# Performance work log

Measured on AMD Instinct MI355X. Metric: run time of the kernel, lower is better.

## Reference

```python
import jax, jax.numpy as jnp
import numpy as np

LX = LZ = 64
B_BOND = 8
KCH = 3
DX = DZ = 2
N_STATES = 4
SAMPLES = 65536


def setup_inputs() -> dict:
    key = jax.random.key(0)
    k1, k2, k3, k4 = jax.random.split(key, 4)
    biadj = jax.random.normal(k1, (LX, LZ, B_BOND), dtype=jnp.float32)
    eps_ten = jax.random.normal(k2, (B_BOND, KCH, DX, DZ), dtype=jnp.float32)
    chi = jax.random.normal(k3, (N_STATES, N_STATES, KCH), dtype=jnp.float32)
    x0_idx = jax.random.randint(k4, (SAMPLES, LX * DX), 0, N_STATES)
    return {"biadj": biadj, "eps_ten": eps_ten, "chi": chi, "x0_idx": x0_idx}


def _kernel(biadj, eps_ten, chi):
    # biadj: [Lx,Lz,b], eps_ten: [b,k,dx,dz], chi: [n,n,k]
    Lx, Lz, _ = biadj.shape
    _, k, dx, dz = eps_ten.shape
    coupling = jnp.tensordot(biadj, eps_ten, axes=([2], [0]))  # [Lx,Lz,k,dx,dz]
    coupling = coupling.transpose(0, 3, 1, 4, 2).reshape(Lx * dx, Lz * dz, k)
    return jnp.tensordot(coupling, chi, axes=([2], [2]))  # [X,Z,n,n]


def reference(biadj, eps_ten, chi, x0_idx):
    """ERBM.cd_x with steps=1: one Gibbs sweep + CD loss. Returns (loss, x)."""
    n = chi.shape[0]
    K = _kernel(biadj, eps_ten, chi)  # [X,Z,n,n]
    x0 = jax.nn.one_hot(x0_idx, n, dtype=K.dtype)  # [S,X,n]
    kz, kx = jax.random.split(jax.random.key(42))
    # ez = tensordot(x0, K, dims=([1,2],[0,2])) -> [S,Z,n]
    ez = jnp.einsum('sxa,xzab->szb', x0, K)
    z = jax.nn.one_hot(jax.random.categorical(kz, -ez), n, dtype=K.dtype)
    # ex = tensordot(z, K, dims=([1,2],[1,3])) -> [S,X,n]
    ex = jnp.einsum('szb,xzab->sxa', z, K)
    x = jax.nn.one_hot(jax.random.categorical(kx, -ex), n, dtype=K.dtype)
    loss = jnp.sum(ex * (x0 - x), axis=(1, 2)).mean()
    return loss, x
```

## Files before the change

kernel.cpp:

```cpp
#include <hip/hip_runtime.h>
#include <stdint.h>

#define NS   65536
#define XD   128
#define ZD   128

struct U2 { uint32_t x, y; };

__host__ __device__ constexpr uint32_t rotl32(uint32_t v, int r) {
  return (v << r) | (v >> (32 - r));
}

__host__ __device__ constexpr U2 threefry2x32(uint32_t k0, uint32_t k1,
                                              uint32_t x0, uint32_t x1) {
  uint32_t ks0 = k0, ks1 = k1, ks2 = k0 ^ k1 ^ 0x1BD11BDAu;
  x0 += ks0; x1 += ks1;
  x0 += x1; x1 = rotl32(x1, 13); x1 ^= x0;
  x0 += x1; x1 = rotl32(x1, 15); x1 ^= x0;
  x0 += x1; x1 = rotl32(x1, 26); x1 ^= x0;
  x0 += x1; x1 = rotl32(x1,  6); x1 ^= x0;
  x0 += ks1; x1 += ks2 + 1u;
  x0 += x1; x1 = rotl32(x1, 17); x1 ^= x0;
  x0 += x1; x1 = rotl32(x1, 29); x1 ^= x0;
  x0 += x1; x1 = rotl32(x1, 16); x1 ^= x0;
  x0 += x1; x1 = rotl32(x1, 24); x1 ^= x0;
  x0 += ks2; x1 += ks0 + 2u;
  x0 += x1; x1 = rotl32(x1, 13); x1 ^= x0;
  x0 += x1; x1 = rotl32(x1, 15); x1 ^= x0;
  x0 += x1; x1 = rotl32(x1, 26); x1 ^= x0;
  x0 += x1; x1 = rotl32(x1,  6); x1 ^= x0;
  x0 += ks0; x1 += ks1 + 3u;
  x0 += x1; x1 = rotl32(x1, 17); x1 ^= x0;
  x0 += x1; x1 = rotl32(x1, 29); x1 ^= x0;
  x0 += x1; x1 = rotl32(x1, 16); x1 ^= x0;
  x0 += x1; x1 = rotl32(x1, 24); x1 ^= x0;
  x0 += ks1; x1 += ks2 + 4u;
  x0 += x1; x1 = rotl32(x1, 13); x1 ^= x0;
  x0 += x1; x1 = rotl32(x1, 15); x1 ^= x0;
  x0 += x1; x1 = rotl32(x1, 26); x1 ^= x0;
  x0 += x1; x1 = rotl32(x1,  6); x1 ^= x0;
  x0 += ks2; x1 += ks0 + 5u;
  return {x0, x1};
}

constexpr U2 KEYZ = threefry2x32(0u, 42u, 0u, 0u);
constexpr U2 KEYX = threefry2x32(0u, 42u, 0u, 1u);
constexpr uint32_t KZ0 = KEYZ.x, KZ1 = KEYZ.y;
constexpr uint32_t KX0 = KEYX.x, KX1 = KEYX.y;

__device__ inline float gumbel32f(uint32_t k0, uint32_t k1, uint32_t idx) {
  U2 h = threefry2x32(k0, k1, 0u, idx);
  uint32_t bits = h.x ^ h.y;
  float f = __uint_as_float((bits >> 9) | 0x3f800000u) - 1.0f;
  float u = fmaxf(f, 1.1754943508222875e-38f);
  float lu = __logf(u);
  return -__logf(-lu);
}

__global__ __launch_bounds__(256) void pack_x0(const int* __restrict__ x0,
                                               uint32_t* __restrict__ pk,
                                               double* __restrict__ loss_acc) {
  int t = blockIdx.x * 256 + threadIdx.x;
  if (t == 0) *loss_acc = 0.0;
  const int4* src = (const int4*)x0 + (size_t)t * 4;
  uint32_t w = 0;
#pragma unroll
  for (int i = 0; i < 4; ++i) {
    int4 v = src[i];
    w |= (uint32_t)(v.x & 3) << (8 * i + 0);
    w |= (uint32_t)(v.y & 3) << (8 * i + 2);
    w |= (uint32_t)(v.z & 3) << (8 * i + 4);
    w |= (uint32_t)(v.w & 3) << (8 * i + 6);
  }
  pk[t] = w;
}

__global__ __launch_bounds__(256) void build_k(const float* __restrict__ biadj,
                                               const float* __restrict__ eps,
                                               const float* __restrict__ chi,
                                               float* __restrict__ Kz,
                                               float* __restrict__ Kx) {
  int t = blockIdx.x * 256 + threadIdx.x;
  int xx = t >> 7, zz = t & 127;
  int ix = xx >> 1, dx = xx & 1;
  int iz = zz >> 1, dz = zz & 1;
  double c0 = 0.0, c1 = 0.0, c2 = 0.0;
#pragma unroll
  for (int b = 0; b < 8; ++b) {
    double bi = (double)biadj[(ix * 64 + iz) * 8 + b];
    c0 += bi * (double)eps[((b * 3 + 0) * 2 + dx) * 2 + dz];
    c1 += bi * (double)eps[((b * 3 + 1) * 2 + dx) * 2 + dz];
    c2 += bi * (double)eps[((b * 3 + 2) * 2 + dx) * 2 + dz];
  }
#pragma unroll
  for (int p = 0; p < 4; ++p)
#pragma unroll
    for (int q = 0; q < 4; ++q) {
      double kv = c0 * (double)chi[(p * 4 + q) * 3 + 0]
                + c1 * (double)chi[(p * 4 + q) * 3 + 1]
                + c2 * (double)chi[(p * 4 + q) * 3 + 2];
      float kf = (float)kv;
      Kz[((zz * 128 + xx) * 4 + p) * 4 + q] = kf;
      Kx[((xx * 128 + zz) * 4 + q) * 4 + p] = kf;
    }
}

__global__ __launch_bounds__(256) void build_pairs(const float* __restrict__ Kz,
                                                   const float* __restrict__ Kx,
                                                   float4* __restrict__ PZ,
                                                   float4* __restrict__ PX) {
  int gid = blockIdx.x * 256 + threadIdx.x;
  int isX = gid >> 17;
  int t = gid & 131071;
  int c = t & 15, rp = (t >> 4) & 63, r = t >> 10;
  const float4* K4 = (const float4*)(isX ? Kx : Kz);
  float4 kA = K4[(r * 128 + 2 * rp) * 4 + (c & 3)];
  float4 kB = K4[(r * 128 + 2 * rp + 1) * 4 + (c >> 2)];
  float4* P = isX ? PX : PZ;
  P[(r * 64 + rp) * 16 + c] =
      float4{kA.x + kB.x, kA.y + kB.y, kA.z + kB.z, kA.w + kB.w};
}

__device__ inline void pair_accum2(const float4* __restrict__ L,
                                   const uint32_t* __restrict__ cw,
                                   double* __restrict__ dA,
                                   double* __restrict__ dB) {
#pragma unroll
  for (int g = 0; g < 4; ++g) {
    float a0 = 0.f, a1 = 0.f, a2 = 0.f, a3 = 0.f;
    float b0 = 0.f, b1 = 0.f, b2 = 0.f, b3 = 0.f;
#pragma unroll
    for (int j2 = 0; j2 < 2; ++j2) {
      uint32_t w = cw[2 * g + j2];
#pragma unroll
      for (int t = 0; t < 8; ++t) {
        int c = (w >> (4 * t)) & 15;
        const float4* e = &L[(16 * g + 8 * j2 + t) * 16 + c];
        float4 e0 = e[0];
        float4 e1 = e[1024];
        a0 += e0.x; a1 += e0.y; a2 += e0.z; a3 += e0.w;
        b0 += e1.x; b1 += e1.y; b2 += e1.z; b3 += e1.w;
      }
    }
    dA[0] += (double)a0; dA[1] += (double)a1; dA[2] += (double)a2; dA[3] += (double)a3;
    dB[0] += (double)b0; dB[1] += (double)b1; dB[2] += (double)b2; dB[3] += (double)b3;
  }
}

__device__ inline int argmax4(double v0, double v1, double v2, double v3) {
  int best = 0; double bv = v0;
  if (v1 > bv) { bv = v1; best = 1; }
  if (v2 > bv) { bv = v2; best = 2; }
  if (v3 > bv) { bv = v3; best = 3; }
  return best;
}

__global__ __launch_bounds__(256, 4) void ez_pair(const float4* __restrict__ PZ,
                                                  const uint32_t* __restrict__ pk,
                                                  uint8_t* __restrict__ zidxT) {
  __shared__ float4 Ltab[2048];
  int tid = threadIdx.x;
  int by = blockIdx.y;
  {
    const uint4* src = (const uint4*)(PZ + (size_t)by * 2048);
    uint4* dst = (uint4*)Ltab;
#pragma unroll
    for (int i = 0; i < 8; ++i) dst[tid + i * 256] = src[tid + i * 256];
  }
  __syncthreads();
  int s = blockIdx.x * 256 + tid;
  uint32_t cw[8];
  {
    uint4 w0 = *(const uint4*)(pk + (size_t)s * 8);
    uint4 w1 = *(const uint4*)(pk + (size_t)s * 8 + 4);
    cw[0] = w0.x; cw[1] = w0.y; cw[2] = w0.z; cw[3] = w0.w;
    cw[4] = w1.x; cw[5] = w1.y; cw[6] = w1.z; cw[7] = w1.w;
  }
  double dA[4] = {0, 0, 0, 0}, dB[4] = {0, 0, 0, 0};
  pair_accum2(Ltab, cw, dA, dB);

  int z0 = 2 * by, z1 = 2 * by + 1;
  uint32_t ibA = ((uint32_t)s * 128u + (uint32_t)z0) * 4u;
  int bestA = argmax4((double)gumbel32f(KZ0, KZ1, ibA + 0u) - dA[0],
                      (double)gumbel32f(KZ0, KZ1, ibA + 1u) - dA[1],
                      (double)gumbel32f(KZ0, KZ1, ibA + 2u) - dA[2],
                      (double)gumbel32f(KZ0, KZ1, ibA + 3u) - dA[3]);
  uint32_t ibB = ibA + 4u;
  int bestB = argmax4((double)gumbel32f(KZ0, KZ1, ibB + 0u) - dB[0],
                      (double)gumbel32f(KZ0, KZ1, ibB + 1u) - dB[1],
                      (double)gumbel32f(KZ0, KZ1, ibB + 2u) - dB[2],
                      (double)gumbel32f(KZ0, KZ1, ibB + 3u) - dB[3]);
  zidxT[(size_t)z0 * NS + s] = (uint8_t)bestA;
  zidxT[(size_t)z1 * NS + s] = (uint8_t)bestB;
}

__global__ __launch_bounds__(256) void repack_z(const uint8_t* __restrict__ zidxT,
                                                uint32_t* __restrict__ zpk) {
  uint32_t t = blockIdx.x * 256u + threadIdx.x;
  uint32_t j = t >> 16, s = t & 65535u;
  uint32_t w = 0;
#pragma unroll
  for (int k = 0; k < 16; ++k)
    w |= (uint32_t)zidxT[(size_t)(16 * j + k) * NS + s] << (2 * k);
  zpk[t] = w;
}

__global__ __launch_bounds__(256, 4) void ex_pair(const float4* __restrict__ PX,
                                                  const uint32_t* __restrict__ zpk,
                                                  const uint32_t* __restrict__ pk,
                                                  uint8_t* __restrict__ xidxT,
                                                  double* __restrict__ loss_acc) {
  __shared__ float4 Ltab[2048];
  __shared__ double red[4];
  int tid = threadIdx.x;
  int by = blockIdx.y;
  {
    const uint4* src = (const uint4*)(PX + (size_t)by * 2048);
    uint4* dst = (uint4*)Ltab;
#pragma unroll
    for (int i = 0; i < 8; ++i) dst[tid + i * 256] = src[tid + i * 256];
  }
  __syncthreads();
  int s = blockIdx.x * 256 + tid;
  uint32_t cw[8];
#pragma unroll
  for (int j = 0; j < 8; ++j) cw[j] = zpk[(size_t)j * NS + s];
  double dA[4] = {0, 0, 0, 0}, dB[4] = {0, 0, 0, 0};
  pair_accum2(Ltab, cw, dA, dB);

  int x0 = 2 * by, x1 = 2 * by + 1;
  uint32_t ibA = ((uint32_t)s * 128u + (uint32_t)x0) * 4u;
  int bestA = argmax4((double)gumbel32f(KX0, KX1, ibA + 0u) - dA[0],
                      (double)gumbel32f(KX0, KX1, ibA + 1u) - dA[1],
                      (double)gumbel32f(KX0, KX1, ibA + 2u) - dA[2],
                      (double)gumbel32f(KX0, KX1, ibA + 3u) - dA[3]);
  uint32_t ibB = ibA + 4u;
  int bestB = argmax4((double)gumbel32f(KX0, KX1, ibB + 0u) - dB[0],
                      (double)gumbel32f(KX0, KX1, ibB + 1u) - dB[1],
                      (double)gumbel32f(KX0, KX1, ibB + 2u) - dB[2],
                      (double)gumbel32f(KX0, KX1, ibB + 3u) - dB[3]);
  xidxT[(size_t)x0 * NS + s] = (uint8_t)bestA;
  xidxT[(size_t)x1 * NS + s] = (uint8_t)bestB;

  uint32_t wj = pk[(size_t)s * 8 + (x0 >> 4)];
  int aiA = (wj >> (2 * (x0 & 15))) & 3;
  int aiB = (wj >> (2 * (x1 & 15))) & 3;
  double term =
      ((aiA == 0) ? dA[0] : (aiA == 1) ? dA[1] : (aiA == 2) ? dA[2] : dA[3]) -
      ((bestA == 0) ? dA[0] : (bestA == 1) ? dA[1] : (bestA == 2) ? dA[2] : dA[3]) +
      ((aiB == 0) ? dB[0] : (aiB == 1) ? dB[1] : (aiB == 2) ? dB[2] : dB[3]) -
      ((bestB == 0) ? dB[0] : (bestB == 1) ? dB[1] : (bestB == 2) ? dB[2] : dB[3]);
#pragma unroll
  for (int off = 32; off > 0; off >>= 1) term += __shfl_down(term, off, 64);
  int wid = tid >> 6;
  if ((tid & 63) == 0) red[wid] = term;
  __syncthreads();
  if (tid == 0) atomicAdd(loss_acc, red[0] + red[1] + red[2] + red[3]);
}

__global__ __launch_bounds__(256) void write_out(const uint8_t* __restrict__ xidxT,
                                                 const double* __restrict__ loss_acc,
                                                 float* __restrict__ out) {
  __shared__ uint8_t tile[128 * 80];
  int tid = threadIdx.x;
  int s0 = blockIdx.x * 64;
  {
    int x = tid >> 1, chunk = tid & 1;
    const uint8_t* src = xidxT + (size_t)x * NS + s0 + chunk * 32;
    uint4 v0 = *(const uint4*)(src);
    uint4 v1 = *(const uint4*)(src + 16);
    *(uint4*)&tile[x * 80 + chunk * 32 + 0]  = v0;
    *(uint4*)&tile[x * 80 + chunk * 32 + 16] = v1;
  }
  __syncthreads();
  float* dst = out + 1 + (size_t)s0 * 512;
#pragma unroll 4
  for (int k = 0; k < 128; ++k) {
    int f = k * 256 + tid;
    int c = f & 3, x = (f >> 2) & 127, sl = f >> 9;
    uint8_t b = tile[x * 80 + sl];
    dst[f] = (c == (int)b) ? 1.0f : 0.0f;
  }
  if (blockIdx.x == 0 && tid == 0) out[0] = (float)(*loss_acc * (1.0 / 65536.0));
}

extern "C" void kernel_launch(void* const* d_in, const int* in_sizes, int n_in,
                              void* d_out, int out_size, void* d_ws, size_t ws_size,
                              hipStream_t stream) {
  const float* biadj = (const float*)d_in[0];
  const float* eps   = (const float*)d_in[1];
  const float* chi   = (const float*)d_in[2];
  const int*   x0    = (const int*)d_in[3];
  float* out = (float*)d_out;

  char* w = (char*)d_ws;
  double*   loss_acc = (double*)w;                 w += 256;
  float*    Kz    = (float*)w;                     w += (size_t)128 * 128 * 16 * 4;
  float*    Kx    = (float*)w;                     w += (size_t)128 * 128 * 16 * 4;
  uint32_t* pk    = (uint32_t*)w;                  w += (size_t)NS * 8 * 4;
  uint8_t*  zidxT = (uint8_t*)w;                   w += (size_t)NS * ZD;
  uint32_t* zpk   = (uint32_t*)w;                  w += (size_t)NS * 8 * 4;
  uint8_t*  xidxT = (uint8_t*)w;                   w += (size_t)NS * XD;
  float4*   PZ    = (float4*)w;                    w += (size_t)128 * 64 * 16 * 16;
  float4*   PX    = (float4*)w;

  pack_x0<<<NS * 8 / 256, 256, 0, stream>>>(x0, pk, loss_acc);
  build_k<<<64, 256, 0, stream>>>(biadj, eps, chi, Kz, Kx);
  build_pairs<<<1024, 256, 0, stream>>>(Kz, Kx, PZ, PX);
  ez_pair<<<dim3(NS / 256, ZD / 2), 256, 0, stream>>>(PZ, pk, zidxT);
  repack_z<<<NS * 8 / 256, 256, 0, stream>>>(zidxT, zpk);
  ex_pair<<<dim3(NS / 256, XD / 2), 256, 0, stream>>>(PX, zpk, pk, xidxT, loss_acc);
  write_out<<<NS / 64, 256, 0, stream>>>(xidxT, loss_acc, out);
}
```

Baseline: 540.4 us.

## Process two samples per thread in pair kernels and fuse init kernels

The ez_pair and ex_pair kernels now handle two samples per thread, halving the grid so each block's shared-memory table load is amortized over twice as many samples. The x0 packing and K building kernels are merged into one launch, and the per-block loss reduction now does one atomic per wavefront instead of a shared-memory sync. This adds register pressure from doubled accumulators, and the min-blocks hint is raised to 5, which could cause spills, and more contended double atomics.

```diff
diff --git a/kernel.cpp b/kernel.cpp
--- a/kernel.cpp
+++ b/kernel.cpp
@@ -57,52 +57,53 @@
   return -__logf(-lu);
 }
 
-__global__ __launch_bounds__(256) void pack_x0(const int* __restrict__ x0,
-                                               uint32_t* __restrict__ pk,
-                                               double* __restrict__ loss_acc) {
-  int t = blockIdx.x * 256 + threadIdx.x;
-  if (t == 0) *loss_acc = 0.0;
-  const int4* src = (const int4*)x0 + (size_t)t * 4;
-  uint32_t w = 0;
-#pragma unroll
-  for (int i = 0; i < 4; ++i) {
-    int4 v = src[i];
-    w |= (uint32_t)(v.x & 3) << (8 * i + 0);
-    w |= (uint32_t)(v.y & 3) << (8 * i + 2);
-    w |= (uint32_t)(v.z & 3) << (8 * i + 4);
-    w |= (uint32_t)(v.w & 3) << (8 * i + 6);
-  }
-  pk[t] = w;
-}
-
-__global__ __launch_bounds__(256) void build_k(const float* __restrict__ biadj,
-                                               const float* __restrict__ eps,
-                                               const float* __restrict__ chi,
-                                               float* __restrict__ Kz,
-                                               float* __restrict__ Kx) {
-  int t = blockIdx.x * 256 + threadIdx.x;
-  int xx = t >> 7, zz = t & 127;
-  int ix = xx >> 1, dx = xx & 1;
-  int iz = zz >> 1, dz = zz & 1;
-  double c0 = 0.0, c1 = 0.0, c2 = 0.0;
-#pragma unroll
-  for (int b = 0; b < 8; ++b) {
-    double bi = (double)biadj[(ix * 64 + iz) * 8 + b];
-    c0 += bi * (double)eps[((b * 3 + 0) * 2 + dx) * 2 + dz];
-    c1 += bi * (double)eps[((b * 3 + 1) * 2 + dx) * 2 + dz];
-    c2 += bi * (double)eps[((b * 3 + 2) * 2 + dx) * 2 + dz];
-  }
-#pragma unroll
-  for (int p = 0; p < 4; ++p)
-#pragma unroll
-    for (int q = 0; q < 4; ++q) {
-      double kv = c0 * (double)chi[(p * 4 + q) * 3 + 0]
-                + c1 * (double)chi[(p * 4 + q) * 3 + 1]
-                + c2 * (double)chi[(p * 4 + q) * 3 + 2];
-      float kf = (float)kv;
-      Kz[((zz * 128 + xx) * 4 + p) * 4 + q] = kf;
-      Kx[((xx * 128 + zz) * 4 + q) * 4 + p] = kf;
+__global__ __launch_bounds__(256) void init_fused(const int* __restrict__ x0,
+                                                  const float* __restrict__ biadj,
+                                                  const float* __restrict__ eps,
+                                                  const float* __restrict__ chi,
+                                                  uint32_t* __restrict__ pk,
+                                                  float* __restrict__ Kz,
+                                                  float* __restrict__ Kx,
+                                                  double* __restrict__ loss_acc) {
+  if (blockIdx.x < 2048) {
+    int t = blockIdx.x * 256 + threadIdx.x;
+    if (t == 0) *loss_acc = 0.0;
+    const int4* src = (const int4*)x0 + (size_t)t * 4;
+    uint32_t w = 0;
+#pragma unroll
+    for (int i = 0; i < 4; ++i) {
+      int4 v = src[i];
+      w |= (uint32_t)(v.x & 3) << (8 * i + 0);
+      w |= (uint32_t)(v.y & 3) << (8 * i + 2);
+      w |= (uint32_t)(v.z & 3) << (8 * i + 4);
+      w |= (uint32_t)(v.w & 3) << (8 * i + 6);
     }
+    pk[t] = w;
+  } else {
+    int t = (blockIdx.x - 2048) * 256 + threadIdx.x;
+    int xx = t >> 7, zz = t & 127;
+    int ix = xx >> 1, dx = xx & 1;
+    int iz = zz >> 1, dz = zz & 1;
+    double c0 = 0.0, c1 = 0.0, c2 = 0.0;
+#pragma unroll
+    for (int b = 0; b < 8; ++b) {
+      double bi = (double)biadj[(ix * 64 + iz) * 8 + b];
+      c0 += bi * (double)eps[((b * 3 + 0) * 2 + dx) * 2 + dz];
+      c1 += bi * (double)eps[((b * 3 + 1) * 2 + dx) * 2 + dz];
+      c2 += bi * (double)eps[((b * 3 + 2) * 2 + dx) * 2 + dz];
+    }
+#pragma unroll
+    for (int p = 0; p < 4; ++p)
+#pragma unroll
+      for (int q = 0; q < 4; ++q) {
+        double kv = c0 * (double)chi[(p * 4 + q) * 3 + 0]
+                  + c1 * (double)chi[(p * 4 + q) * 3 + 1]
+                  + c2 * (double)chi[(p * 4 + q) * 3 + 2];
+        float kf = (float)kv;
+        Kz[((zz * 128 + xx) * 4 + p) * 4 + q] = kf;
+        Kx[((xx * 128 + zz) * 4 + q) * 4 + p] = kf;
+      }
+  }
 }
 
 __global__ __launch_bounds__(256) void build_pairs(const float* __restrict__ Kz,
@@ -121,29 +122,43 @@
       float4{kA.x + kB.x, kA.y + kB.y, kA.z + kB.z, kA.w + kB.w};
 }
 
-__device__ inline void pair_accum2(const float4* __restrict__ L,
-                                   const uint32_t* __restrict__ cw,
-                                   double* __restrict__ dA,
-                                   double* __restrict__ dB) {
+__device__ inline void pair_accum4(const float4* __restrict__ L,
+                                   const uint32_t* __restrict__ cw0,
+                                   const uint32_t* __restrict__ cw1,
+                                   double* __restrict__ d0A, double* __restrict__ d0B,
+                                   double* __restrict__ d1A, double* __restrict__ d1B) {
 #pragma unroll
   for (int g = 0; g < 4; ++g) {
-    float a0 = 0.f, a1 = 0.f, a2 = 0.f, a3 = 0.f;
-    float b0 = 0.f, b1 = 0.f, b2 = 0.f, b3 = 0.f;
+    float a0[4] = {0.f, 0.f, 0.f, 0.f};
+    float b0[4] = {0.f, 0.f, 0.f, 0.f};
+    float a1[4] = {0.f, 0.f, 0.f, 0.f};
+    float b1[4] = {0.f, 0.f, 0.f, 0.f};
 #pragma unroll
     for (int j2 = 0; j2 < 2; ++j2) {
-      uint32_t w = cw[2 * g + j2];
+      uint32_t w0 = cw0[2 * g + j2];
+      uint32_t w1 = cw1[2 * g + j2];
 #pragma unroll
       for (int t = 0; t < 8; ++t) {
-        int c = (w >> (4 * t)) & 15;
-        const float4* e = &L[(16 * g + 8 * j2 + t) * 16 + c];
-        float4 e0 = e[0];
-        float4 e1 = e[1024];
-        a0 += e0.x; a1 += e0.y; a2 += e0.z; a3 += e0.w;
-        b0 += e1.x; b1 += e1.y; b2 += e1.z; b3 += e1.w;
+        int base = (16 * g + 8 * j2 + t) * 16;
+        int c0 = (w0 >> (4 * t)) & 15;
+        int c1 = (w1 >> (4 * t)) & 15;
+        const float4* e0 = &L[base + c0];
+        const float4* e1 = &L[base + c1];
+        float4 e00 = e0[0];
+        float4 e01 = e0[1024];
+        float4 e10 = e1[0];
+        float4 e11 = e1[1024];
+        a0[0] += e00.x; a0[1] += e00.y; a0[2] += e00.z; a0[3] += e00.w;
+        b0[0] += e01.x; b0[1] += e01.y; b0[2] += e01.z; b0[3] += e01.w;
+        a1[0] += e10.x; a1[1] += e10.y; a1[2] += e10.z; a1[3] += e10.w;
+        b1[0] += e11.x; b1[1] += e11.y; b1[2] += e11.z; b1[3] += e11.w;
       }
     }
-    dA[0] += (double)a0; dA[1] += (double)a1; dA[2] += (double)a2; dA[3] += (double)a3;
-    dB[0] += (double)b0; dB[1] += (double)b1; dB[2] += (double)b2; dB[3] += (double)b3;
+#pragma unroll
+    for (int k = 0; k < 4; ++k) {
+      d0A[k] += (double)a0[k]; d0B[k] += (double)b0[k];
+      d1A[k] += (double)a1[k]; d1B[k] += (double)b1[k];
+    }
   }
 }
 
@@ -155,7 +170,15 @@
   return best;
 }
 
-__global__ __launch_bounds__(256, 4) void ez_pair(const float4* __restrict__ PZ,
+__device__ inline int sample4(uint32_t k0, uint32_t k1, uint32_t ib,
+                              const double* d) {
+  return argmax4((double)gumbel32f(k0, k1, ib + 0u) - d[0],
+                 (double)gumbel32f(k0, k1, ib + 1u) - d[1],
+                 (double)gumbel32f(k0, k1, ib + 2u) - d[2],
+                 (double)gumbel32f(k0, k1, ib + 3u) - d[3]);
+}
+
+__global__ __launch_bounds__(256, 5) void ez_pair(const float4* __restrict__ PZ,
                                                   const uint32_t* __restrict__ pk,
                                                   uint8_t* __restrict__ zidxT) {
   __shared__ float4 Ltab[2048];
@@ -168,30 +191,30 @@
     for (int i = 0; i < 8; ++i) dst[tid + i * 256] = src[tid + i * 256];
   }
   __syncthreads();
-  int s = blockIdx.x * 256 + tid;
-  uint32_t cw[8];
+  int s0 = blockIdx.x * 512 + tid;
+  int s1 = s0 + 256;
+  uint32_t cw0[8], cw1[8];
   {
-    uint4 w0 = *(const uint4*)(pk + (size_t)s * 8);
-    uint4 w1 = *(const uint4*)(pk + (size_t)s * 8 + 4);
-    cw[0] = w0.x; cw[1] = w0.y; cw[2] = w0.z; cw[3] = w0.w;
-    cw[4] = w1.x; cw[5] = w1.y; cw[6] = w1.z; cw[7] = w1.w;
-  }
-  double dA[4] = {0, 0, 0, 0}, dB[4] = {0, 0, 0, 0};
-  pair_accum2(Ltab, cw, dA, dB);
+    uint4 w0 = *(const uint4*)(pk + (size_t)s0 * 8);
+    uint4 w1 = *(const uint4*)(pk + (size_t)s0 * 8 + 4);
+    cw0[0] = w0.x; cw0[1] = w0.y; cw0[2] = w0.z; cw0[3] = w0.w;
+    cw0[4] = w1.x; cw0[5] = w1.y; cw0[6] = w1.z; cw0[7] = w1.w;
+    uint4 w2 = *(const uint4*)(pk + (size_t)s1 * 8);
+    uint4 w3 = *(const uint4*)(pk + (size_t)s1 * 8 + 4);
+    cw1[0] = w2.x; cw1[1] = w2.y; cw1[2] = w2.z; cw1[3] = w2.w;
+    cw1[4] = w3.x; cw1[5] = w3.y; cw1[6] = w3.z; cw1[7] = w3.w;
+  }
+  double d0A[4] = {0, 0, 0, 0}, d0B[4] = {0, 0, 0, 0};
+  double d1A[4] = {0, 0, 0, 0}, d1B[4] = {0, 0, 0, 0};
+  pair_accum4(Ltab, cw0, cw1, d0A, d0B, d1A, d1B);
 
   int z0 = 2 * by, z1 = 2 * by + 1;
-  uint32_t ibA = ((uint32_t)s * 128u + (uint32_t)z0) * 4u;
-  int bestA = argmax4((double)gumbel32f(KZ0, KZ1, ibA + 0u) - dA[0],
-                      (double)gumbel32f(KZ0, KZ1, ibA + 1u) - dA[1],
-                      (double)gumbel32f(KZ0, KZ1, ibA + 2u) - dA[2],
-                      (double)gumbel32f(KZ0, KZ1, ibA + 3u) - dA[3]);
-  uint32_t ibB = ibA + 4u;
-  int bestB = argmax4((double)gumbel32f(KZ0, KZ1, ibB + 0u) - dB[0],
-                      (double)gumbel32f(KZ0, KZ1, ibB + 1u) - dB[1],
-                      (double)gumbel32f(KZ0, KZ1, ibB + 2u) - dB[2],
-                      (double)gumbel32f(KZ0, KZ1, ibB + 3u) - dB[3]);
-  zidxT[(size_t)z0 * NS + s] = (uint8_t)bestA;
-  zidxT[(size_t)z1 * NS + s] = (uint8_t)bestB;
+  uint32_t ib0 = ((uint32_t)s0 * 128u + (uint32_t)z0) * 4u;
+  uint32_t ib1 = ((uint32_t)s1 * 128u + (uint32_t)z0) * 4u;
+  zidxT[(size_t)z0 * NS + s0] = (uint8_t)sample4(KZ0, KZ1, ib0, d0A);
+  zidxT[(size_t)z1 * NS + s0] = (uint8_t)sample4(KZ0, KZ1, ib0 + 4u, d0B);
+  zidxT[(size_t)z0 * NS + s1] = (uint8_t)sample4(KZ0, KZ1, ib1, d1A);
+  zidxT[(size_t)z1 * NS + s1] = (uint8_t)sample4(KZ0, KZ1, ib1 + 4u, d1B);
 }
 
 __global__ __launch_bounds__(256) void repack_z(const uint8_t* __restrict__ zidxT,
@@ -205,13 +228,12 @@
   zpk[t] = w;
 }
 
-__global__ __launch_bounds__(256, 4) void ex_pair(const float4* __restrict__ PX,
+__global__ __launch_bounds__(256, 5) void ex_pair(const float4* __restrict__ PX,
                                                   const uint32_t* __restrict__ zpk,
                                                   const uint32_t* __restrict__ pk,
                                                   uint8_t* __restrict__ xidxT,
                                                   double* __restrict__ loss_acc) {
   __shared__ float4 Ltab[2048];
-  __shared__ double red[4];
   int tid = threadIdx.x;
   int by = blockIdx.y;
   {
@@ -221,41 +243,41 @@
     for (int i = 0; i < 8; ++i) dst[tid + i * 256] = src[tid + i * 256];
   }
   __syncthreads();
-  int s = blockIdx.x * 256 + tid;
-  uint32_t cw[8];
-#pragma unroll
-  for (int j = 0; j < 8; ++j) cw[j] = zpk[(size_t)j * NS + s];
-  double dA[4] = {0, 0, 0, 0}, dB[4] = {0, 0, 0, 0};
-  pair_accum2(Ltab, cw, dA, dB);
+  int s0 = blockIdx.x * 512 + tid;
+  int s1 = s0 + 256;
+  uint32_t cw0[8], cw1[8];
+#pragma unroll
+  for (int j = 0; j < 8; ++j) {
+    cw0[j] = zpk[(size_t)j * NS + s0];
+    cw1[j] = zpk[(size_t)j * NS + s1];
+  }
+  double d0A[4] = {0, 0, 0, 0}, d0B[4] = {0, 0, 0, 0};
+  double d1A[4] = {0, 0, 0, 0}, d1B[4] = {0, 0, 0, 0};
+  pair_accum4(Ltab, cw0, cw1, d0A, d0B, d1A, d1B);
 
   int x0 = 2 * by, x1 = 2 * by + 1;
-  uint32_t ibA = ((uint32_t)s * 128u + (uint32_t)x0) * 4u;
-  int bestA = argmax4((double)gumbel32f(KX0, KX1, ibA + 0u) - dA[0],
-                      (double)gumbel32f(KX0, KX1, ibA + 1u) - dA[1],
-                      (double)gumbel32f(KX0, KX1, ibA + 2u) - dA[2],
-                      (double)gumbel32f(KX0, KX1, ibA + 3u) - dA[3]);
-  uint32_t ibB = ibA + 4u;
-  int bestB = argmax4((double)gumbel32f(KX0, KX1, ibB + 0u) - dB[0],
-                      (double)gumbel32f(KX0, KX1, ibB + 1u) - dB[1],
-                      (double)gumbel32f(KX0, KX1, ibB + 2u) - dB[2],
-                      (double)gumbel32f(KX0, KX1, ibB + 3u) - dB[3]);
-  xidxT[(size_t)x0 * NS + s] = (uint8_t)bestA;
-  xidxT[(size_t)x1 * NS + s] = (uint8_t)bestB;
-
-  uint32_t wj = pk[(size_t)s * 8 + (x0 >> 4)];
-  int aiA = (wj >> (2 * (x0 & 15))) & 3;
-  int aiB = (wj >> (2 * (x1 & 15))) & 3;
-  double term =
-      ((aiA == 0) ? dA[0] : (aiA == 1) ? dA[1] : (aiA == 2) ? dA[2] : dA[3]) -
-      ((bestA == 0) ? dA[0] : (bestA == 1) ? dA[1] : (bestA == 2) ? dA[2] : dA[3]) +
-      ((aiB == 0) ? dB[0] : (aiB == 1) ? dB[1] : (aiB == 2) ? dB[2] : dB[3]) -
-      ((bestB == 0) ? dB[0] : (bestB == 1) ? dB[1] : (bestB == 2) ? dB[2] : dB[3]);
+  uint32_t ib0 = ((uint32_t)s0 * 128u + (uint32_t)x0) * 4u;
+  uint32_t ib1 = ((uint32_t)s1 * 128u + (uint32_t)x0) * 4u;
+  int b0A = sample4(KX0, KX1, ib0, d0A);
+  int b0B = sample4(KX0, KX1, ib0 + 4u, d0B);
+  int b1A = sample4(KX0, KX1, ib1, d1A);
+  int b1B = sample4(KX0, KX1, ib1 + 4u, d1B);
+  xidxT[(size_t)x0 * NS + s0] = (uint8_t)b0A;
+  xidxT[(size_t)x1 * NS + s0] = (uint8_t)b0B;
+  xidxT[(size_t)x0 * NS + s1] = (uint8_t)b1A;
+  xidxT[(size_t)x1 * NS + s1] = (uint8_t)b1B;
+
+  uint32_t w0 = pk[(size_t)s0 * 8 + (x0 >> 4)];
+  uint32_t w1 = pk[(size_t)s1 * 8 + (x0 >> 4)];
+  int ai0A = (w0 >> (2 * (x0 & 15))) & 3;
+  int ai0B = (w0 >> (2 * (x1 & 15))) & 3;
+  int ai1A = (w1 >> (2 * (x0 & 15))) & 3;
+  int ai1B = (w1 >> (2 * (x1 & 15))) & 3;
+  double term = d0A[ai0A] - d0A[b0A] + d0B[ai0B] - d0B[b0B]
+              + d1A[ai1A] - d1A[b1A] + d1B[ai1B] - d1B[b1B];
 #pragma unroll
   for (int off = 32; off > 0; off >>= 1) term += __shfl_down(term, off, 64);
-  int wid = tid >> 6;
-  if ((tid & 63) == 0) red[wid] = term;
-  __syncthreads();
-  if (tid == 0) atomicAdd(loss_acc, red[0] + red[1] + red[2] + red[3]);
+  if ((tid & 63) == 0) atomicAdd(loss_acc, term);
 }
 
 __global__ __launch_bounds__(256) void write_out(const uint8_t* __restrict__ xidxT,
@@ -304,11 +326,10 @@
   float4*   PZ    = (float4*)w;                    w += (size_t)128 * 64 * 16 * 16;
   float4*   PX    = (float4*)w;
 
-  pack_x0<<<NS * 8 / 256, 256, 0, stream>>>(x0, pk, loss_acc);
-  build_k<<<64, 256, 0, stream>>>(biadj, eps, chi, Kz, Kx);
+  init_fused<<<2112, 256, 0, stream>>>(x0, biadj, eps, chi, pk, Kz, Kx, loss_acc);
   build_pairs<<<1024, 256, 0, stream>>>(Kz, Kx, PZ, PX);
-  ez_pair<<<dim3(NS / 256, ZD / 2), 256, 0, stream>>>(PZ, pk, zidxT);
+  ez_pair<<<dim3(NS / 512, ZD / 2), 256, 0, stream>>>(PZ, pk, zidxT);
   repack_z<<<NS * 8 / 256, 256, 0, stream>>>(zidxT, zpk);
-  ex_pair<<<dim3(NS / 256, XD / 2), 256, 0, stream>>>(PX, zpk, pk, xidxT, loss_acc);
+  ex_pair<<<dim3(NS / 512, XD / 2), 256, 0, stream>>>(PX, zpk, pk, xidxT, loss_acc);
   write_out<<<NS / 64, 256, 0, stream>>>(xidxT, loss_acc, out);
 }
```

After: 743.5 us. +37.6%, slower.
